# Optimization experiments

Measured on AMD Instinct MI355X. Metric: run time of the kernel, lower is better.

## Reference

```python
import jax, jax.numpy as jnp
import numpy as np

D, NH, HD, NL, NP, DFF = 256, 8, 32, 4, 4, 1024
B, LQ = 16, 900
SHAPES = np.array([[100, 100], [50, 50], [25, 25], [13, 13]], dtype=np.int64)
_AREAS = SHAPES[:, 0] * SHAPES[:, 1]
LSI = np.concatenate([[0], np.cumsum(_AREAS)[:-1]]).astype(np.int64)
S = int(_AREAS.sum())  # 13294


def setup_inputs() -> dict:
    key = jax.random.key(0)
    ki = iter(jax.random.split(key, 40))
    def nrm(shape, s=1.0):
        return jax.random.normal(next(ki), shape, jnp.float32) * s
    p = dict(
        tgt=nrm((B, LQ, D)),
        query_pos=nrm((B, LQ, D)) * 0.1,
        reference_points=jax.random.uniform(next(ki), (B, LQ, NL, 2), jnp.float32),
        src=nrm((B, S, D)),
        src_spatial_shapes=SHAPES,
        level_start_index=LSI,
        src_padding_mask=np.zeros((B, S), dtype=bool),
        Wq=nrm((D, D), 0.02), bq=jnp.zeros((D,)),
        Wk=nrm((D, D), 0.02), bk=jnp.zeros((D,)),
        Wv=nrm((D, D), 0.02), bv=jnp.zeros((D,)),
        Wo=nrm((D, D), 0.02), bo=jnp.zeros((D,)),
        g2=jnp.ones((D,)), be2=jnp.zeros((D,)),
        Woff=nrm((D, NH * NL * NP * 2), 0.02),
        boff=jax.random.uniform(next(ki), (NH * NL * NP * 2,), jnp.float32, -0.5, 0.5),
        Waw=nrm((D, NH * NL * NP), 0.02), baw=jnp.zeros((NH * NL * NP,)),
        Wval=nrm((D, D), 0.02), bval=jnp.zeros((D,)),
        Wout=nrm((D, D), 0.02), bout=jnp.zeros((D,)),
        g1=jnp.ones((D,)), be1=jnp.zeros((D,)),
        W1f=nrm((D, DFF), 0.02), b1f=jnp.zeros((DFF,)),
        W2f=nrm((DFF, D), 0.02), b2f=jnp.zeros((D,)),
        g3=jnp.ones((D,)), be3=jnp.zeros((D,)),
    )
    return p


def layernorm(x, g, b):
    m = jnp.mean(x, -1, keepdims=True)
    v = jnp.var(x, -1, keepdims=True)
    return (x - m) * jax.lax.rsqrt(v + 1e-5) * g + b


def reference(tgt, query_pos, reference_points, src, src_spatial_shapes,
              level_start_index, src_padding_mask,
              Wq, bq, Wk, bk, Wv, bv, Wo, bo, g2, be2,
              Woff, boff, Waw, baw, Wval, bval, Wout, bout, g1, be1,
              W1f, b1f, W2f, b2f, g3, be3):
    Bq, Lq, _ = tgt.shape
    # ---- self-attention (q = k = tgt + pos, v = tgt), dropout in eval = identity
    q = tgt + query_pos
    qh = (q @ Wq + bq).reshape(Bq, Lq, NH, HD)
    kh = (q @ Wk + bk).reshape(Bq, Lq, NH, HD)
    vh = (tgt @ Wv + bv).reshape(Bq, Lq, NH, HD)
    att = jax.nn.softmax(jnp.einsum('bqhd,bkhd->bhqk', qh, kh) / np.sqrt(HD), axis=-1)
    sa = jnp.einsum('bhqk,bkhd->bqhd', att, vh).reshape(Bq, Lq, D) @ Wo + bo
    tgt = layernorm(tgt + sa, g2, be2)
    # ---- multi-scale deformable cross-attention
    query = tgt + query_pos
    value = src @ Wval + bval
    value = jnp.where(jnp.asarray(src_padding_mask)[..., None], 0.0, value)
    value = value.reshape(Bq, -1, NH, HD)
    off = (query @ Woff + boff).reshape(Bq, Lq, NH, NL, NP, 2)
    aw = jax.nn.softmax((query @ Waw + baw).reshape(Bq, Lq, NH, NL * NP), axis=-1)
    aw = aw.reshape(Bq, Lq, NH, NL, NP)
    ss = np.asarray(src_spatial_shapes)
    lsi = np.asarray(level_start_index)
    norm = jnp.asarray(ss[:, ::-1].astype(np.float32))  # (W, H) per level
    # sampling locations in [0,1]: [B, Lq, NH, NL, NP, 2]
    loc = reference_points[:, :, None, :, None, :] + off / norm[None, None, None, :, None, :]
    out = jnp.zeros((Bq, NH, Lq, HD), value.dtype)
    for l in range(NL):
        Hc, Wc = int(ss[l, 0]), int(ss[l, 1])
        v2 = value[:, lsi[l]:lsi[l] + Hc * Wc].transpose(0, 2, 1, 3)  # [B, NH, H*W, HD]
        x = loc[:, :, :, l, :, 0] * Wc - 0.5  # [B, Lq, NH, NP] (align_corners=False)
        y = loc[:, :, :, l, :, 1] * Hc - 0.5
        x0 = jnp.floor(x); y0 = jnp.floor(y)
        lx = x - x0; ly = y - y0
        x0i = x0.astype(jnp.int32); y0i = y0.astype(jnp.int32)
        samp = jnp.zeros((Bq, NH, Lq * NP, HD), value.dtype)
        for dy, dx, w in ((0, 0, (1 - ly) * (1 - lx)), (0, 1, (1 - ly) * lx),
                          (1, 0, ly * (1 - lx)), (1, 1, ly * lx)):
            xi = x0i + dx; yi = y0i + dy
            valid = (xi >= 0) & (xi < Wc) & (yi >= 0) & (yi < Hc)  # zero padding
            idx = jnp.clip(yi, 0, Hc - 1) * Wc + jnp.clip(xi, 0, Wc - 1)
            idx2 = idx.transpose(0, 2, 1, 3).reshape(Bq, NH, Lq * NP)
            g = jnp.take_along_axis(v2, idx2[..., None], axis=2)  # [B, NH, Lq*NP, HD]
            wv = (w * valid).transpose(0, 2, 1, 3).reshape(Bq, NH, Lq * NP)
            samp = samp + wv[..., None] * g
        samp = samp.reshape(Bq, NH, Lq, NP, HD)
        out = out + jnp.einsum('bqhp,bhqpd->bhqd', aw[:, :, :, l, :], samp)
    ca = out.transpose(0, 2, 1, 3).reshape(Bq, Lq, D) @ Wout + bout
    tgt = layernorm(tgt + ca, g1, be1)
    # ---- FFN
    ff = jax.nn.relu(tgt @ W1f + b1f) @ W2f + b2f
    return layernorm(tgt + ff, g3, be3)
```

## Files before the change

### kernel.cpp

```cpp
#include <hip/hip_runtime.h>
#include <math.h>

#define DD 256
#define NH 8
#define HD 32
#define NL 4
#define NP 4
#define DFF 1024
#define BB 16
#define LQ 900
#define S_TOT 13294

#define M1   (BB * LQ)
#define MP1  14464
#define MV   (BB * S_TOT)
#define MPV  212736

typedef unsigned short u16;
typedef unsigned int   u32;
typedef __attribute__((ext_vector_type(8))) short s8v;
typedef __attribute__((ext_vector_type(4))) float f32x4;

__constant__ int c_H[NL]    = {100, 50, 25, 13};
__constant__ int c_W[NL]    = {100, 50, 25, 13};
__constant__ int c_base[NL] = {0, 10000, 12500, 13125};

__device__ __forceinline__ float b2f(u16 u) {
    return __uint_as_float(((u32)u) << 16);
}
__device__ __forceinline__ u16 f2b(float f) {
    u32 x = __float_as_uint(f);
    u32 r = x + 0x7fffu + ((x >> 16) & 1u);
    return (u16)(r >> 16);
}
__device__ __forceinline__ u32 pk2(float a, float b) {
    return (u32)f2b(a) | ((u32)f2b(b) << 16);
}
__device__ __forceinline__ void gload16(const u16* g, u16* ldsbase) {
    __builtin_amdgcn_global_load_lds(
        (const __attribute__((address_space(1))) unsigned int*)(const void*)g,
        (__attribute__((address_space(3))) unsigned int*)(void*)ldsbase,
        16, 0, 0);
}

#define OFF_QK   0
#define OFF_V    131072
#define OFF_O    196608
#define OFF_VAL  262144
#define OFF_OUT  327680
#define OFF_OA   393216
#define OFF_F1   491520
#define OFF_F2   753664
#define WTS_TOT  1015808

__global__ __launch_bounds__(256)
void prep_kernel(const float* __restrict__ Wq, const float* __restrict__ Wk,
                 const float* __restrict__ Wv, const float* __restrict__ Wo,
                 const float* __restrict__ Wval, const float* __restrict__ Wout,
                 const float* __restrict__ Woff, const float* __restrict__ Waw,
                 const float* __restrict__ W1f, const float* __restrict__ W2f,
                 const float* __restrict__ pbq, const float* __restrict__ pbk,
                 const float* __restrict__ boff, const float* __restrict__ baw,
                 u16* __restrict__ WTS, float* __restrict__ bqk, float* __restrict__ boa)
{
    int t = blockIdx.x;
    if (t >= 992) {
        if (t == 992) {
            for (int i = threadIdx.x; i < 512; i += 256)
                bqk[i] = (i < 256) ? pbq[i] : pbk[i - 256];
        } else {
            for (int i = threadIdx.x; i < 384; i += 256)
                boa[i] = (i < 256) ? boff[i] : baw[i - 256];
        }
        return;
    }
    const float* src; u16* dst; int K, N, tt;
    if (t < 448) {
        int wsel = t >> 6; tt = t & 63;
        const float* srcs[7] = {Wq, Wk, Wv, Wo, Wval, Wout, Woff};
        const int   offs[7]  = {OFF_QK, OFF_QK + 65536, OFF_V, OFF_O, OFF_VAL, OFF_OUT, OFF_OA};
        src = srcs[wsel]; dst = WTS + offs[wsel]; K = 256; N = 256;
    } else if (t < 480) {
        tt = t - 448; src = Waw; dst = WTS + OFF_OA + 65536; K = 256; N = 128;
    } else if (t < 736) {
        tt = t - 480; src = W1f; dst = WTS + OFF_F1; K = 256; N = 1024;
    } else {
        tt = t - 736; src = W2f; dst = WTS + OFF_F2; K = 1024; N = 256;
    }
    int nt = N / 32;
    int n0 = (tt % nt) * 32, k0 = (tt / nt) * 32;

    __shared__ float tb[32][33];
    int tx = threadIdx.x & 31, ty = threadIdx.x >> 5;
    #pragma unroll
    for (int i = 0; i < 4; ++i) {
        int k = ty + i * 8;
        tb[k][tx] = src[(size_t)(k0 + k) * N + n0 + tx];
    }
    __syncthreads();
    #pragma unroll
    for (int i = 0; i < 4; ++i) {
        int n = ty + i * 8;
        dst[(size_t)(n0 + n) * K + k0 + tx] = f2b(tb[tx][n]);
    }
}

__global__ __launch_bounds__(256)
void acvt2_kernel(const float* __restrict__ tgt, const float* __restrict__ qpos,
                  u16* __restrict__ B0, u16* __restrict__ B1)
{
    int i8 = blockIdx.x * 256 + threadIdx.x;
    int row = i8 >> 5;
    uint4 o0, o1;
    if (row < M1) {
        const float4* tp = (const float4*)(tgt + (size_t)i8 * 8);
        const float4* pp = (const float4*)(qpos + (size_t)i8 * 8);
        float4 t0 = tp[0], t1 = tp[1], p0 = pp[0], p1 = pp[1];
        o1.x = pk2(t0.x, t0.y); o1.y = pk2(t0.z, t0.w);
        o1.z = pk2(t1.x, t1.y); o1.w = pk2(t1.z, t1.w);
        o0.x = pk2(t0.x + p0.x, t0.y + p0.y); o0.y = pk2(t0.z + p0.z, t0.w + p0.w);
        o0.z = pk2(t1.x + p1.x, t1.y + p1.y); o0.w = pk2(t1.z + p1.z, t1.w + p1.w);
    } else {
        o0.x = o0.y = o0.z = o0.w = 0;
        o1 = o0;
    }
    ((uint4*)B0)[i8] = o0;
    ((uint4*)B1)[i8] = o1;
}

template<int BNT, int OUTBF, int RELU>
__global__ __launch_bounds__(256)
void mgemm(const u16* __restrict__ A, const u16* __restrict__ Bt,
           const float* __restrict__ bias, void* __restrict__ Cv,
           int K, int N, int Mreal)
{
    constexpr int MF = (BNT == 128) ? 4 : 2;
    __shared__ u16 Asu[2][128 * 32];
    __shared__ u16 Bsu[2][BNT * 32];

    int tid = threadIdx.x;
    int w = tid >> 6, l = tid & 63;
    int mbase = (BNT == 128) ? (w >> 1) * 64 : w * 32;
    int nbase = (BNT == 128) ? (w & 1) * 64 : 0;
    long m0 = (long)blockIdx.y * 128;
    int n0 = blockIdx.x * BNT;

    f32x4 acc[MF][4];
    #pragma unroll
    for (int i = 0; i < MF; ++i)
        #pragma unroll
        for (int j = 0; j < 4; ++j) {
            acc[i][j][0] = 0.f; acc[i][j][1] = 0.f;
            acc[i][j][2] = 0.f; acc[i][j][3] = 0.f;
        }

    int lr = l & 15, lk = (l >> 4) * 8;
    int srow = l >> 2;
    int scol = (l & 3) * 8;

    auto stage = [&](int buf, int k0) {
        if (BNT == 128) {
            #pragma unroll
            for (int j = 0; j < 2; ++j) {
                int row = w * 32 + j * 16;
                gload16(Bt + (size_t)(n0 + row + srow) * K + k0 + scol, &Bsu[buf][row * 32]);
            }
        } else {
            int row = w * 16;
            gload16(Bt + (size_t)(n0 + row + srow) * K + k0 + scol, &Bsu[buf][row * 32]);
        }
        #pragma unroll
        for (int j = 0; j < 2; ++j) {
            int row = w * 32 + j * 16;
            gload16(A + (m0 + row + srow) * (long)K + k0 + scol, &Asu[buf][row * 32]);
        }
    };

    int nsteps = K >> 5;
    stage(0, 0);
    __syncthreads();

    int cur = 0;
    for (int s = 0; s < nsteps; ++s) {
        if (s + 1 < nsteps) stage(cur ^ 1, (s + 1) * 32);
        s8v af[MF], bf[4];
        #pragma unroll
        for (int mi = 0; mi < MF; ++mi)
            af[mi] = *(const s8v*)(Asu[cur] + (mbase + mi * 16 + lr) * 32 + lk);
        #pragma unroll
        for (int nj = 0; nj < 4; ++nj)
            bf[nj] = *(const s8v*)(Bsu[cur] + (nbase + nj * 16 + lr) * 32 + lk);
        #pragma unroll
        for (int mi = 0; mi < MF; ++mi)
            #pragma unroll
            for (int nj = 0; nj < 4; ++nj)
                acc[mi][nj] = __builtin_amdgcn_mfma_f32_16x16x32_bf16(
                    af[mi], bf[nj], acc[mi][nj], 0, 0, 0);
        __syncthreads();
        cur ^= 1;
    }

    int lq = l >> 4;
    #pragma unroll
    for (int nj = 0; nj < 4; ++nj) {
        int col = n0 + nbase + nj * 16 + lr;
        float bv = bias[col];
        #pragma unroll
        for (int mi = 0; mi < MF; ++mi) {
            #pragma unroll
            for (int r = 0; r < 4; ++r) {
                long row = m0 + mbase + mi * 16 + lq * 4 + r;
                float v = acc[mi][nj][r] + bv;
                if (RELU) v = fmaxf(v, 0.f);
                if (OUTBF) ((u16*)Cv)[row * N + col] = f2b(v);
                else       ((float*)Cv)[row * N + col] = v;
            }
        }
    }
}

__global__ __launch_bounds__(256)
void vgemm(const float* __restrict__ A, const u16* __restrict__ Bt,
           const float* __restrict__ bias, u16* __restrict__ C, int Mreal)
{
    const int K = 256, N = 256;
    __shared__ u16 Asu[128 * 32];
    __shared__ u16 Bsu[128 * 32];

    int tid = threadIdx.x;
    int w = tid >> 6, l = tid & 63;
    int wr = w >> 1, wc = w & 1;
    long m0 = (long)blockIdx.y * 128;
    int n0 = blockIdx.x * 128;

    f32x4 acc[4][4];
    #pragma unroll
    for (int i = 0; i < 4; ++i)
        #pragma unroll
        for (int j = 0; j < 4; ++j) {
            acc[i][j][0] = 0.f; acc[i][j][1] = 0.f;
            acc[i][j][2] = 0.f; acc[i][j][3] = 0.f;
        }

    int lr = l & 15, lk = (l >> 4) * 8;
    int srow = l >> 2, scol = (l & 3) * 8;

    for (int k0 = 0; k0 < K; k0 += 32) {
        #pragma unroll
        for (int j = 0; j < 2; ++j) {
            int row = w * 32 + j * 16;
            gload16(Bt + (size_t)(n0 + row + srow) * K + k0 + scol, &Bsu[row * 32]);
        }
        int c = tid;
        #pragma unroll
        for (int it = 0; it < 4; ++it) {
            int row = c >> 3, col = (c & 7) * 4;
            long gr = m0 + row;
            if (gr >= Mreal) gr = Mreal - 1;
            float4 v = *(const float4*)(A + gr * K + k0 + col);
            ushort4 o;
            o.x = f2b(v.x); o.y = f2b(v.y); o.z = f2b(v.z); o.w = f2b(v.w);
            ((ushort4*)Asu)[c] = o;
            c += 256;
        }
        __syncthreads();
        s8v af[4], bf[4];
        #pragma unroll
        for (int mi = 0; mi < 4; ++mi)
            af[mi] = *(const s8v*)(Asu + (wr * 64 + mi * 16 + lr) * 32 + lk);
        #pragma unroll
        for (int nj = 0; nj < 4; ++nj)
            bf[nj] = *(const s8v*)(Bsu + (wc * 64 + nj * 16 + lr) * 32 + lk);
        #pragma unroll
        for (int mi = 0; mi < 4; ++mi)
            #pragma unroll
            for (int nj = 0; nj < 4; ++nj)
                acc[mi][nj] = __builtin_amdgcn_mfma_f32_16x16x32_bf16(
                    af[mi], bf[nj], acc[mi][nj], 0, 0, 0);
        __syncthreads();
    }

    int lq = l >> 4;
    #pragma unroll
    for (int nj = 0; nj < 4; ++nj) {
        int col = n0 + wc * 64 + nj * 16 + lr;
        float bv = bias[col];
        #pragma unroll
        for (int mi = 0; mi < 4; ++mi) {
            #pragma unroll
            for (int r = 0; r < 4; ++r) {
                long row = m0 + wr * 64 + mi * 16 + lq * 4 + r;
                C[row * N + col] = f2b(acc[mi][nj][r] + bv);
            }
        }
    }
}

#define QT 64
#define KT2 64
#define KSP 48
#define VSP 40
#define PSP 72
__global__ __launch_bounds__(256)
void mattn(const u16* __restrict__ qk, const u16* __restrict__ vh,
           u16* __restrict__ sa)
{
    __shared__ u16 Ks[KT2][KSP];
    __shared__ u32 Vt32[32][VSP];
    __shared__ u16 Ps[4][16][PSP];

    int tid = threadIdx.x;
    int w = tid >> 6, l = tid & 63;
    int lr = l & 15, hi = l >> 4;
    int b = blockIdx.x >> 3, h = blockIdx.x & 7;
    int q0 = blockIdx.y * QT + w * 16;

    s8v qf;
    {
        s8v raw = *(const s8v*)(qk + ((size_t)(b * LQ + q0 + lr) * 512) + h * HD + hi * 8);
        #pragma unroll
        for (int j = 0; j < 8; ++j)
            raw[j] = (short)f2b(b2f((u16)raw[j]) * 0.17677669529663687f);
        qf = raw;
    }

    f32x4 o0 = {0.f,0.f,0.f,0.f}, o1 = {0.f,0.f,0.f,0.f};
    float lrun[4] = {0.f,0.f,0.f,0.f};

    const u16* kbase = qk + (size_t)b * LQ * 512 + 256 + h * HD;
    const u16* vbase = vh + (size_t)b * LQ * 256 + h * HD;

    int krow = tid >> 2, kc8 = (tid & 3) * 8;
    int k2 = tid & 31, d0 = (tid >> 5) * 4;

    for (int kb = 0; kb < LQ; kb += KT2) {
        int gk = kb + krow;        if (gk >= LQ) gk = LQ - 1;
        int gv0 = kb + 2 * k2;     if (gv0 >= LQ) gv0 = LQ - 1;
        int gv1 = kb + 2 * k2 + 1; if (gv1 >= LQ) gv1 = LQ - 1;
        uint4 kv = *(const uint4*)(kbase + (size_t)gk * 512 + kc8);
        uint2 va = *(const uint2*)(vbase + (size_t)gv0 * 256 + d0);
        uint2 vb = *(const uint2*)(vbase + (size_t)gv1 * 256 + d0);
        __syncthreads();
        *(uint4*)(&Ks[krow][kc8]) = kv;
        Vt32[d0 + 0][k2] = (va.x & 0xffffu)      | (vb.x << 16);
        Vt32[d0 + 1][k2] = (va.x >> 16)          | (vb.x & 0xffff0000u);
        Vt32[d0 + 2][k2] = (va.y & 0xffffu)      | (vb.y << 16);
        Vt32[d0 + 3][k2] = (va.y >> 16)          | (vb.y & 0xffff0000u);
        __syncthreads();

        f32x4 s[4];
        #pragma unroll
        for (int kk = 0; kk < 4; ++kk) {
            s8v bk = *(const s8v*)(&Ks[kk * 16 + lr][hi * 8]);
            f32x4 z = {0.f,0.f,0.f,0.f};
            s[kk] = __builtin_amdgcn_mfma_f32_16x16x32_bf16(qf, bk, z, 0, 0, 0);
        }
        if (kb + KT2 > LQ) {
            #pragma unroll
            for (int kk = 0; kk < 4; ++kk)
                if (kb + kk * 16 + lr >= LQ) {
                    s[kk][0] = -1e30f; s[kk][1] = -1e30f;
                    s[kk][2] = -1e30f; s[kk][3] = -1e30f;
                }
        }

        #pragma unroll
        for (int r = 0; r < 4; ++r) {
            float p0 = __expf(s[0][r]);
            float p1 = __expf(s[1][r]);
            float p2 = __expf(s[2][r]);
            float p3 = __expf(s[3][r]);
            lrun[r] += (p0 + p1) + (p2 + p3);
            int qr = hi * 4 + r;
            Ps[w][qr][lr]      = f2b(p0);
            Ps[w][qr][16 + lr] = f2b(p1);
            Ps[w][qr][32 + lr] = f2b(p2);
            Ps[w][qr][48 + lr] = f2b(p3);
        }

        s8v ap0  = *(const s8v*)(&Ps[w][lr][hi * 8]);
        s8v ap1  = *(const s8v*)(&Ps[w][lr][32 + hi * 8]);
        s8v bv00 = *(const s8v*)(&Vt32[lr][hi * 4]);
        s8v bv10 = *(const s8v*)(&Vt32[lr][16 + hi * 4]);
        s8v bv01 = *(const s8v*)(&Vt32[16 + lr][hi * 4]);
        s8v bv11 = *(const s8v*)(&Vt32[16 + lr][16 + hi * 4]);
        o0 = __builtin_amdgcn_mfma_f32_16x16x32_bf16(ap0, bv00, o0, 0, 0, 0);
        o0 = __builtin_amdgcn_mfma_f32_16x16x32_bf16(ap1, bv10, o0, 0, 0, 0);
        o1 = __builtin_amdgcn_mfma_f32_16x16x32_bf16(ap0, bv01, o1, 0, 0, 0);
        o1 = __builtin_amdgcn_mfma_f32_16x16x32_bf16(ap1, bv11, o1, 0, 0, 0);
    }

    #pragma unroll
    for (int r = 0; r < 4; ++r) {
        float ps = lrun[r];
        ps += __shfl_xor(ps, 1);
        ps += __shfl_xor(ps, 2);
        ps += __shfl_xor(ps, 4);
        ps += __shfl_xor(ps, 8);
        int q = q0 + hi * 4 + r;
        if (q < LQ) {
            float inv = 1.f / ps;
            u16* op = sa + (size_t)(b * LQ + q) * DD + h * HD;
            op[lr]      = f2b(o0[r] * inv);
            op[16 + lr] = f2b(o1[r] * inv);
        }
    }
}

__global__ __launch_bounds__(256)
void ln_kernel(const float* __restrict__ x, const u16* __restrict__ y,
               const float* __restrict__ g, const float* __restrict__ be,
               float* __restrict__ out, const float* __restrict__ pos,
               u16* __restrict__ bfout, int M)
{
    int wave = threadIdx.x >> 6;
    int lane = threadIdx.x & 63;
    int row = blockIdx.x * 4 + wave;
    if (row >= M) return;
    float4 xv = ((const float4*)(x + (size_t)row * DD))[lane];
    ushort4 yv = ((const ushort4*)(y + (size_t)row * DD))[lane];
    float v[4] = {xv.x + b2f(yv.x), xv.y + b2f(yv.y),
                  xv.z + b2f(yv.z), xv.w + b2f(yv.w)};
    float s = v[0] + v[1] + v[2] + v[3];
    float sq = v[0]*v[0] + v[1]*v[1] + v[2]*v[2] + v[3]*v[3];
    for (int o = 32; o; o >>= 1) {
        s += __shfl_xor(s, o);
        sq += __shfl_xor(sq, o);
    }
    float mean = s * (1.f / DD);
    float var = sq * (1.f / DD) - mean * mean;
    float r = rsqrtf(var + 1e-5f);
    float4 gv = ((const float4*)g)[lane];
    float4 bv = ((const float4*)be)[lane];
    float4 ov;
    ov.x = (v[0] - mean) * r * gv.x + bv.x;
    ov.y = (v[1] - mean) * r * gv.y + bv.y;
    ov.z = (v[2] - mean) * r * gv.z + bv.z;
    ov.w = (v[3] - mean) * r * gv.w + bv.w;
    ((float4*)(out + (size_t)row * DD))[lane] = ov;
    if (bfout) {
        float4 pv = make_float4(0.f, 0.f, 0.f, 0.f);
        if (pos) pv = ((const float4*)(pos + (size_t)row * DD))[lane];
        ushort4 bo;
        bo.x = f2b(ov.x + pv.x); bo.y = f2b(ov.y + pv.y);
        bo.z = f2b(ov.z + pv.z); bo.w = f2b(ov.w + pv.w);
        ((ushort4*)(bfout + (size_t)row * DD))[lane] = bo;
    }
}

__global__ __launch_bounds__(256)
void sample_kernel(const float* __restrict__ offaw, const float* __restrict__ refp,
                   const u16* __restrict__ value, u16* __restrict__ out)
{
    __shared__ float2 sPW[2][128][4];
    int t = threadIdx.x;
    int sub = t >> 7;
    int bq = blockIdx.x * 2 + sub;
    int b = bq / LQ;

    {
        int pt = t & 127;
        int h = pt >> 4, j = pt & 15, l = j >> 2, p = j & 3;
        const float* row = offaw + (size_t)bq * 384;
        float lg = row[256 + h * 16 + j];
        float mx = lg;
        mx = fmaxf(mx, __shfl_xor(mx, 1));
        mx = fmaxf(mx, __shfl_xor(mx, 2));
        mx = fmaxf(mx, __shfl_xor(mx, 4));
        mx = fmaxf(mx, __shfl_xor(mx, 8));
        float e = __expf(lg - mx);
        float se = e;
        se += __shfl_xor(se, 1);
        se += __shfl_xor(se, 2);
        se += __shfl_xor(se, 4);
        se += __shfl_xor(se, 8);
        float aw = e / se;

        float ox = row[h * 32 + l * 8 + p * 2 + 0];
        float oy = row[h * 32 + l * 8 + p * 2 + 1];
        int Hc = c_H[l], Wc = c_W[l];
        float x = refp[(size_t)bq * 8 + l * 2 + 0] * Wc + ox - 0.5f;
        float y = refp[(size_t)bq * 8 + l * 2 + 1] * Hc + oy - 0.5f;
        float x0f = floorf(x), y0f = floorf(y);
        float lx = x - x0f, ly = y - y0f;
        int x0 = (int)x0f, y0 = (int)y0f;
        int vb = (b * S_TOT + c_base[l]) * 128;
        #pragma unroll
        for (int c = 0; c < 4; ++c) {
            int dy = c >> 1, dx = c & 1;
            int xi = x0 + dx, yi = y0 + dy;
            bool ok = (xi >= 0) & (xi < Wc) & (yi >= 0) & (yi < Hc);
            float wgt = (dy ? ly : 1.f - ly) * (dx ? lx : 1.f - lx) * aw;
            float2 pw;
            pw.x = __int_as_float(ok ? vb + (yi * Wc + xi) * 128 : 0);
            pw.y = ok ? wgt : 0.f;
            sPW[sub][pt][c] = pw;
        }
    }
    __syncthreads();

    {
        int s = t & 127;
        int h = s >> 4, d2 = s & 15;
        const u32* v32 = (const u32*)value;
        int lane = h * 16 + d2;
        float a0 = 0.f, a1 = 0.f;
        #pragma unroll
        for (int j = 0; j < 16; ++j) {
            #pragma unroll
            for (int c = 0; c < 4; ++c) {
                float2 pw = sPW[sub][h * 16 + j][c];
                u32 pv = v32[__float_as_int(pw.x) + lane];
                a0 += pw.y * __uint_as_float(pv << 16);
                a1 += pw.y * __uint_as_float(pv & 0xffff0000u);
            }
        }
        *(u32*)(out + (size_t)bq * DD + h * 32 + d2 * 2) = pk2(a0, a1);
    }
}

extern "C" void kernel_launch(void* const* d_in, const int* in_sizes, int n_in,
                              void* d_out, int out_size, void* d_ws, size_t ws_size,
                              hipStream_t stream)
{
    const float* tgt  = (const float*)d_in[0];
    const float* qpos = (const float*)d_in[1];
    const float* refp = (const float*)d_in[2];
    const float* src  = (const float*)d_in[3];
    const float* Wq  = (const float*)d_in[7];
    const float* pbq = (const float*)d_in[8];
    const float* Wk  = (const float*)d_in[9];
    const float* pbk = (const float*)d_in[10];
    const float* Wv  = (const float*)d_in[11];
    const float* pbv = (const float*)d_in[12];
    const float* Wo  = (const float*)d_in[13];
    const float* pbo = (const float*)d_in[14];
    const float* g2  = (const float*)d_in[15];
    const float* be2 = (const float*)d_in[16];
    const float* Woff = (const float*)d_in[17];
    const float* boff = (const float*)d_in[18];
    const float* Waw  = (const float*)d_in[19];
    const float* baw  = (const float*)d_in[20];
    const float* Wval = (const float*)d_in[21];
    const float* bval = (const float*)d_in[22];
    const float* Wout = (const float*)d_in[23];
    const float* bout = (const float*)d_in[24];
    const float* g1   = (const float*)d_in[25];
    const float* be1  = (const float*)d_in[26];
    const float* W1f  = (const float*)d_in[27];
    const float* b1f  = (const float*)d_in[28];
    const float* W2f  = (const float*)d_in[29];
    const float* b2f_ = (const float*)d_in[30];
    const float* g3   = (const float*)d_in[31];
    const float* be3  = (const float*)d_in[32];

    char* base = (char*)d_ws;
    size_t off = 0;
    auto alloc = [&](size_t bytes) -> void* {
        void* p = base + off;
        off = (off + bytes + 255) & ~(size_t)255;
        return p;
    };
    const size_t AB = (size_t)MP1 * DD * sizeof(u16);
    u16* B0  = (u16*)alloc(AB);
    u16* B1  = (u16*)alloc(AB);
    u16* BQK = (u16*)alloc((size_t)MP1 * 512 * sizeof(u16));
    u16* B4  = (u16*)alloc(AB);
    u16* TMPB= (u16*)alloc(AB);
    u16* FFH = (u16*)alloc((size_t)MP1 * DFF * sizeof(u16));
    u16* VAL = (u16*)alloc((size_t)MPV * DD * sizeof(u16));
    float* F0 = (float*)alloc((size_t)MP1 * 384 * sizeof(float));
    float* F2 = (float*)alloc((size_t)MP1 * DD * sizeof(float));
    float* F3 = (float*)alloc((size_t)MP1 * DD * sizeof(float));
    u16* WTS = (u16*)alloc((size_t)WTS_TOT * sizeof(u16));
    float* bqk = (float*)alloc(512 * sizeof(float));
    float* boa = (float*)alloc(384 * sizeof(float));

    dim3 blk(256);

    prep_kernel<<<dim3(994), blk, 0, stream>>>(
        Wq, Wk, Wv, Wo, Wval, Wout, Woff, Waw, W1f, W2f,
        pbq, pbk, boff, baw, WTS, bqk, boa);

    const int MT = MP1 / 128;
    const dim3 gval(2, MPV / 128);
    const dim3 g512b(8,  MT);
    const dim3 g256b(4,  MT);
    const dim3 g384b(6,  MT);
    const dim3 g1kb(16,  MT);

    acvt2_kernel<<<dim3(MP1 * 32 / 256), blk, 0, stream>>>(tgt, qpos, B0, B1);
    mgemm<64,1,0><<<g512b, blk, 0, stream>>>(B0, WTS + OFF_QK, bqk, BQK, DD, 512, M1);
    mgemm<64,1,0><<<g256b, blk, 0, stream>>>(B1, WTS + OFF_V, pbv, B4, DD, DD, M1);
    mattn<<<dim3(BB * NH, (LQ + QT - 1) / QT), blk, 0, stream>>>(BQK, B4, B0);
    mgemm<64,1,0><<<g256b, blk, 0, stream>>>(B0, WTS + OFF_O, pbo, TMPB, DD, DD, M1);
    ln_kernel<<<dim3(M1 / 4), blk, 0, stream>>>(tgt, TMPB, g2, be2, F2, qpos, B1, M1);

    vgemm<<<gval, blk, 0, stream>>>(src, WTS + OFF_VAL, bval, VAL, MV);
    mgemm<64,0,0><<<g384b, blk, 0, stream>>>(B1, WTS + OFF_OA, boa, F0, DD, 384, M1);
    sample_kernel<<<dim3(M1 / 2), blk, 0, stream>>>(F0, refp, VAL, B4);
    mgemm<64,1,0><<<g256b, blk, 0, stream>>>(B4, WTS + OFF_OUT, bout, TMPB, DD, DD, M1);
    ln_kernel<<<dim3(M1 / 4), blk, 0, stream>>>(F2, TMPB, g1, be1, F3, nullptr, B1, M1);

    mgemm<64,1,1><<<g1kb, blk, 0, stream>>>(B1, WTS + OFF_F1, b1f, FFH, DD, DFF, M1);
    mgemm<64,1,0><<<g256b, blk, 0, stream>>>(FFH, WTS + OFF_F2, b2f_, TMPB, DFF, DD, M1);
    ln_kernel<<<dim3(M1 / 4), blk, 0, stream>>>(F3, TMPB, g3, be3, (float*)d_out, nullptr, nullptr, M1);
}
```

Baseline: 327.8 us.

## Preload full B tile into LDS and stream A directly into MFMA registers

The value-projection GEMM now loads the whole 128x256 weight slice into shared memory once, up front, so the per-k-step barriers go away. The fp32 activation rows are read straight from global memory into registers in MFMA fragment layout, with the next k-slice prefetched one step ahead. This removes the A staging through LDS and the two syncs per iteration. In exchange it uses 64KB of LDS per block, which limits occupancy, and the per-lane A reads are less coalesced, with each lane reading 32 bytes from its own row.

Result: slower. 403.0 us (+22.9%).

```diff
diff --git a/kernel.cpp b/kernel.cpp
--- a/kernel.cpp
+++ b/kernel.cpp
@@ -224,14 +224,26 @@
            const float* __restrict__ bias, u16* __restrict__ C, int Mreal)
 {
     const int K = 256, N = 256;
-    __shared__ u16 Asu[128 * 32];
-    __shared__ u16 Bsu[128 * 32];
+    __shared__ u16 Bsu[8][128 * 32];
 
     int tid = threadIdx.x;
     int w = tid >> 6, l = tid & 63;
     int wr = w >> 1, wc = w & 1;
     long m0 = (long)blockIdx.y * 128;
     int n0 = blockIdx.x * 128;
+    int lr = l & 15, hi = l >> 4;
+    int lk = hi * 8;
+    int srow = l >> 2, scol = (l & 3) * 8;
+
+    #pragma unroll
+    for (int s = 0; s < 8; ++s) {
+        #pragma unroll
+        for (int j = 0; j < 2; ++j) {
+            int row = w * 32 + j * 16;
+            gload16(Bt + (size_t)(n0 + row + srow) * K + s * 32 + scol,
+                    &Bsu[s][row * 32]);
+        }
+    }
 
     f32x4 acc[4][4];
     #pragma unroll
@@ -242,42 +254,62 @@
             acc[i][j][2] = 0.f; acc[i][j][3] = 0.f;
         }
 
-    int lr = l & 15, lk = (l >> 4) * 8;
-    int srow = l >> 2, scol = (l & 3) * 8;
-
-    for (int k0 = 0; k0 < K; k0 += 32) {
-        #pragma unroll
-        for (int j = 0; j < 2; ++j) {
-            int row = w * 32 + j * 16;
-            gload16(Bt + (size_t)(n0 + row + srow) * K + k0 + scol, &Bsu[row * 32]);
-        }
-        int c = tid;
-        #pragma unroll
-        for (int it = 0; it < 4; ++it) {
-            int row = c >> 3, col = (c & 7) * 4;
-            long gr = m0 + row;
-            if (gr >= Mreal) gr = Mreal - 1;
-            float4 v = *(const float4*)(A + gr * K + k0 + col);
-            ushort4 o;
-            o.x = f2b(v.x); o.y = f2b(v.y); o.z = f2b(v.z); o.w = f2b(v.w);
-            ((ushort4*)Asu)[c] = o;
-            c += 256;
-        }
-        __syncthreads();
-        s8v af[4], bf[4];
-        #pragma unroll
-        for (int mi = 0; mi < 4; ++mi)
-            af[mi] = *(const s8v*)(Asu + (wr * 64 + mi * 16 + lr) * 32 + lk);
+    const float* arow0;
+    const float* arow1;
+    const float* arow2;
+    const float* arow3;
+    {
+        long gr0 = m0 + wr * 64 + 0  * 16 + lr; if (gr0 >= Mreal) gr0 = Mreal - 1;
+        long gr1 = m0 + wr * 64 + 1  * 16 + lr; if (gr1 >= Mreal) gr1 = Mreal - 1;
+        long gr2 = m0 + wr * 64 + 2  * 16 + lr; if (gr2 >= Mreal) gr2 = Mreal - 1;
+        long gr3 = m0 + wr * 64 + 3  * 16 + lr; if (gr3 >= Mreal) gr3 = Mreal - 1;
+        arow0 = A + gr0 * K + lk;
+        arow1 = A + gr1 * K + lk;
+        arow2 = A + gr2 * K + lk;
+        arow3 = A + gr3 * K + lk;
+    }
+
+    __syncthreads();
+
+    float4 pa[4][2], pb[4][2];
+    pa[0][0] = *(const float4*)(arow0 + 0); pa[0][1] = *(const float4*)(arow0 + 4);
+    pa[1][0] = *(const float4*)(arow1 + 0); pa[1][1] = *(const float4*)(arow1 + 4);
+    pa[2][0] = *(const float4*)(arow2 + 0); pa[2][1] = *(const float4*)(arow2 + 4);
+    pa[3][0] = *(const float4*)(arow3 + 0); pa[3][1] = *(const float4*)(arow3 + 4);
+
+    #pragma unroll
+    for (int s = 0; s < 8; ++s) {
+        if (s < 7) {
+            int c = (s + 1) * 32;
+            pb[0][0] = *(const float4*)(arow0 + c); pb[0][1] = *(const float4*)(arow0 + c + 4);
+            pb[1][0] = *(const float4*)(arow1 + c); pb[1][1] = *(const float4*)(arow1 + c + 4);
+            pb[2][0] = *(const float4*)(arow2 + c); pb[2][1] = *(const float4*)(arow2 + c + 4);
+            pb[3][0] = *(const float4*)(arow3 + c); pb[3][1] = *(const float4*)(arow3 + c + 4);
+        }
+        s8v af[4];
+        #pragma unroll
+        for (int mi = 0; mi < 4; ++mi) {
+            s8v t;
+            t[0] = (short)f2b(pa[mi][0].x); t[1] = (short)f2b(pa[mi][0].y);
+            t[2] = (short)f2b(pa[mi][0].z); t[3] = (short)f2b(pa[mi][0].w);
+            t[4] = (short)f2b(pa[mi][1].x); t[5] = (short)f2b(pa[mi][1].y);
+            t[6] = (short)f2b(pa[mi][1].z); t[7] = (short)f2b(pa[mi][1].w);
+            af[mi] = t;
+        }
+        s8v bf[4];
         #pragma unroll
         for (int nj = 0; nj < 4; ++nj)
-            bf[nj] = *(const s8v*)(Bsu + (wc * 64 + nj * 16 + lr) * 32 + lk);
+            bf[nj] = *(const s8v*)(&Bsu[s][(wc * 64 + nj * 16 + lr) * 32 + lk]);
         #pragma unroll
         for (int mi = 0; mi < 4; ++mi)
             #pragma unroll
             for (int nj = 0; nj < 4; ++nj)
                 acc[mi][nj] = __builtin_amdgcn_mfma_f32_16x16x32_bf16(
                     af[mi], bf[nj], acc[mi][nj], 0, 0, 0);
-        __syncthreads();
+        #pragma unroll
+        for (int mi = 0; mi < 4; ++mi) {
+            pa[mi][0] = pb[mi][0]; pa[mi][1] = pb[mi][1];
+        }
     }
 
     int lq = l >> 4;
```
